# Kernel tuning notes

Hardware: AMD Instinct MI355X
Metric: run time of the kernel (lower is better)

## Reference

```python
import jax, jax.numpy as jnp
import numpy as np

# anchor encoding indices: [x,y,z,log w,log l,log h,sin,cos,vx,vy,vz]
NUM_HEADS = 8
LN_EPS = 1e-5


def layer_norm(x, g, b):
    mu = jnp.mean(x, axis=-1, keepdims=True)
    var = jnp.var(x, axis=-1, keepdims=True)
    return (x - mu) * jax.lax.rsqrt(var + LN_EPS) * g + b


def align_anchors_to_frame(anchor, Tm):
    # anchor: (..., N, 11), Tm: (..., 4, 4)
    R = Tm[..., :3, :3]
    t = Tm[..., :3, 3]
    center = jnp.einsum('...ij,...nj->...ni', R, anchor[..., 0:3]) + t[..., None, :]
    size = anchor[..., 3:6]
    yaw = jnp.einsum('...ij,...nj->...ni', R[..., :2, :2], anchor[..., 6:8])
    vel = jnp.einsum('...ij,...nj->...ni', R, anchor[..., 8:11])
    return jnp.concatenate([center, size, yaw, vel], axis=-1)


def setup_inputs() -> dict:
    key = jax.random.key(0)
    ks = jax.random.split(key, 12)
    B, T, N, C, E, A = 2, 12, 1024, 256, 256, 11
    inp = {
        'seq_features': jax.random.normal(ks[0], (B, T, N, C), jnp.float32),
        'seq_anchors': jax.random.normal(ks[1], (B, T, N, A), jnp.float32),
        'T_ego_his2cur': jax.random.normal(ks[2], (B, T, 4, 4), jnp.float32),
        'Wf': jax.random.normal(ks[3], (E, C), jnp.float32) * (C ** -0.5),
        'bf': jnp.zeros((E,), jnp.float32),
        'Wa': jax.random.normal(ks[4], (E, A), jnp.float32) * (A ** -0.5),
        'ba': jnp.zeros((E,), jnp.float32),
        'Win': jax.random.normal(ks[5], (3 * E, E), jnp.float32) * (E ** -0.5),
        'bin_': jnp.zeros((3 * E,), jnp.float32),
        'gamma': jnp.ones((E,), jnp.float32),
        'beta': jnp.zeros((E,), jnp.float32),
    }
    return inp


def reference(seq_features, seq_anchors, T_ego_his2cur, Wf, bf, Wa, ba, Win, bin_, gamma, beta):
    B, T, N, C = seq_features.shape
    E = gamma.shape[0]
    H = NUM_HEADS
    D = E // H

    feat_cur = seq_features[:, 1:]    # (B,T-1,N,C)
    feat_prev = seq_features[:, :-1]
    anc_cur = seq_anchors[:, 1:]
    anc_prev = align_anchors_to_frame(seq_anchors[:, :-1], T_ego_his2cur[:, 1:])

    tok_cur = layer_norm(feat_cur @ Wf.T + bf + anc_cur @ Wa.T + ba, gamma, beta)
    tok_prev = layer_norm(feat_prev @ Wf.T + bf + anc_prev @ Wa.T + ba, gamma, beta)

    Wq, Wk = Win[:E], Win[E:2 * E]
    bq, bk = bin_[:E], bin_[E:2 * E]
    scale = np.float32(D) ** np.float32(-0.5)
    q = ((tok_cur @ Wq.T + bq) * scale).reshape(B, T - 1, N, H, D)
    k = (tok_prev @ Wk.T + bk).reshape(B, T - 1, N, H, D)

    scores = jnp.einsum('btnhd,btmhd->bthnm', q, k)  # (B,T-1,H,N,N)
    attn = jax.nn.softmax(scores, axis=-1).mean(axis=2)  # head-averaged weights

    eye = jnp.broadcast_to(jnp.eye(N, dtype=seq_features.dtype), (B, 1, N, N))
    return jnp.concatenate([eye, attn], axis=1)  # (B,T,N,N)
```

## Files before the change

kernel.cpp:

```cpp
#include <hip/hip_runtime.h>
#include <hip/hip_bf16.h>
#include <math.h>

#define LN_EPS 1e-5f

typedef short bf16x8 __attribute__((ext_vector_type(8)));
typedef float f32x4 __attribute__((ext_vector_type(4)));

__device__ inline short f2bf(float f) {
  union { float f; unsigned u; } v; v.f = f;
  unsigned r = v.u + 0x7FFFu + ((v.u >> 16) & 1u);
  return (short)(r >> 16);
}
__device__ inline float bf2f(unsigned short s) {
  union { unsigned u; float f; } v; v.u = ((unsigned)s) << 16;
  return v.f;
}
__device__ inline float fast_exp2(float x) {
#if __has_builtin(__builtin_amdgcn_exp2f)
  return __builtin_amdgcn_exp2f(x);
#else
  return __expf(x * 0.69314718056f);
#endif
}

__global__ __launch_bounds__(256) void gemm_feat(const float* __restrict__ Ap,
    const float* __restrict__ W, const float* __restrict__ bias,
    short* __restrict__ Out)
{
  __shared__ short lda[64][40];
  __shared__ short ldb[64][40];
  const int tid = threadIdx.x;
  const int bm = blockIdx.x * 64, bn = blockIdx.y * 64;
  const int wid = tid >> 6, lane = tid & 63;
  const int quad = lane >> 4, l15 = lane & 15;
  const int wm = (wid & 1) * 32, wn = (wid >> 1) * 32;
  const int srow = tid >> 2, sseg = tid & 3;

  f32x4 z = {0.f, 0.f, 0.f, 0.f};
  f32x4 acc[2][2];
  acc[0][0] = z; acc[0][1] = z; acc[1][0] = z; acc[1][1] = z;

  for (int kk = 0; kk < 256; kk += 32) {
    {
      const float* ap = Ap + (size_t)(bm + srow) * 256 + kk + sseg * 8;
      f32x4 x0 = *(const f32x4*)ap;
      f32x4 x1 = *(const f32x4*)(ap + 4);
      bf16x8 vv;
      vv[0] = f2bf(x0[0]); vv[1] = f2bf(x0[1]); vv[2] = f2bf(x0[2]); vv[3] = f2bf(x0[3]);
      vv[4] = f2bf(x1[0]); vv[5] = f2bf(x1[1]); vv[6] = f2bf(x1[2]); vv[7] = f2bf(x1[3]);
      *(bf16x8*)&lda[srow][sseg * 8] = vv;
    }
    {
      const float* wp = W + (size_t)(bn + srow) * 256 + kk + sseg * 8;
      f32x4 x0 = *(const f32x4*)wp;
      f32x4 x1 = *(const f32x4*)(wp + 4);
      bf16x8 vv;
      vv[0] = f2bf(x0[0]); vv[1] = f2bf(x0[1]); vv[2] = f2bf(x0[2]); vv[3] = f2bf(x0[3]);
      vv[4] = f2bf(x1[0]); vv[5] = f2bf(x1[1]); vv[6] = f2bf(x1[2]); vv[7] = f2bf(x1[3]);
      *(bf16x8*)&ldb[srow][sseg * 8] = vv;
    }
    __syncthreads();
    bf16x8 af0 = *(const bf16x8*)&lda[wm + l15][quad * 8];
    bf16x8 af1 = *(const bf16x8*)&lda[wm + 16 + l15][quad * 8];
    bf16x8 bq0 = *(const bf16x8*)&ldb[wn + l15][quad * 8];
    bf16x8 bq1 = *(const bf16x8*)&ldb[wn + 16 + l15][quad * 8];
    acc[0][0] = __builtin_amdgcn_mfma_f32_16x16x32_bf16(af0, bq0, acc[0][0], 0, 0, 0);
    acc[0][1] = __builtin_amdgcn_mfma_f32_16x16x32_bf16(af0, bq1, acc[0][1], 0, 0, 0);
    acc[1][0] = __builtin_amdgcn_mfma_f32_16x16x32_bf16(af1, bq0, acc[1][0], 0, 0, 0);
    acc[1][1] = __builtin_amdgcn_mfma_f32_16x16x32_bf16(af1, bq1, acc[1][1], 0, 0, 0);
    __syncthreads();
  }

  #pragma unroll
  for (int i = 0; i < 2; ++i)
    #pragma unroll
    for (int j = 0; j < 2; ++j)
      #pragma unroll
      for (int r = 0; r < 4; ++r) {
        int grow = bm + wm + i * 16 + quad * 4 + r;
        int gcol = bn + wn + j * 16 + l15;
        Out[(size_t)grow * 256 + gcol] = f2bf(acc[i][j][r] + bias[gcol]);
      }
}

__global__ __launch_bounds__(256) void gemm_qk(const short* __restrict__ tokc,
    const short* __restrict__ tokp, const float* __restrict__ Win,
    const float* __restrict__ binv, short* __restrict__ qb, short* __restrict__ kb)
{
  const int sel = blockIdx.z;
  const short* Ap = sel ? tokp : tokc;
  const float* W = Win + (size_t)sel * 65536;
  const float* bias = binv + sel * 256;
  const float alpha = sel ? 1.0f : 0.17677669529663687f * 1.4426950408889634f;
  short* Out = sel ? kb : qb;

  __shared__ short lda[64][40];
  __shared__ short ldb[64][40];
  const int tid = threadIdx.x;
  const int bm = blockIdx.x * 64, bn = blockIdx.y * 64;
  const int wid = tid >> 6, lane = tid & 63;
  const int quad = lane >> 4, l15 = lane & 15;
  const int wm = (wid & 1) * 32, wn = (wid >> 1) * 32;
  const int srow = tid >> 2, sseg = tid & 3;

  f32x4 z = {0.f, 0.f, 0.f, 0.f};
  f32x4 acc[2][2];
  acc[0][0] = z; acc[0][1] = z; acc[1][0] = z; acc[1][1] = z;

  for (int kk = 0; kk < 256; kk += 32) {
    *(bf16x8*)&lda[srow][sseg * 8] =
        *(const bf16x8*)(Ap + (size_t)(bm + srow) * 256 + kk + sseg * 8);
    {
      const float* wp = W + (size_t)(bn + srow) * 256 + kk + sseg * 8;
      f32x4 x0 = *(const f32x4*)wp;
      f32x4 x1 = *(const f32x4*)(wp + 4);
      bf16x8 vv;
      vv[0] = f2bf(x0[0]); vv[1] = f2bf(x0[1]); vv[2] = f2bf(x0[2]); vv[3] = f2bf(x0[3]);
      vv[4] = f2bf(x1[0]); vv[5] = f2bf(x1[1]); vv[6] = f2bf(x1[2]); vv[7] = f2bf(x1[3]);
      *(bf16x8*)&ldb[srow][sseg * 8] = vv;
    }
    __syncthreads();
    bf16x8 af0 = *(const bf16x8*)&lda[wm + l15][quad * 8];
    bf16x8 af1 = *(const bf16x8*)&lda[wm + 16 + l15][quad * 8];
    bf16x8 bq0 = *(const bf16x8*)&ldb[wn + l15][quad * 8];
    bf16x8 bq1 = *(const bf16x8*)&ldb[wn + 16 + l15][quad * 8];
    acc[0][0] = __builtin_amdgcn_mfma_f32_16x16x32_bf16(af0, bq0, acc[0][0], 0, 0, 0);
    acc[0][1] = __builtin_amdgcn_mfma_f32_16x16x32_bf16(af0, bq1, acc[0][1], 0, 0, 0);
    acc[1][0] = __builtin_amdgcn_mfma_f32_16x16x32_bf16(af1, bq0, acc[1][0], 0, 0, 0);
    acc[1][1] = __builtin_amdgcn_mfma_f32_16x16x32_bf16(af1, bq1, acc[1][1], 0, 0, 0);
    __syncthreads();
  }

  #pragma unroll
  for (int i = 0; i < 2; ++i)
    #pragma unroll
    for (int j = 0; j < 2; ++j)
      #pragma unroll
      for (int r = 0; r < 4; ++r) {
        int grow = bm + wm + i * 16 + quad * 4 + r;
        int gcol = bn + wn + j * 16 + l15;
        float v = (acc[i][j][r] + bias[gcol]) * alpha;
        int btr = grow >> 10, nn = grow & 1023, h = gcol >> 5, d = gcol & 31;
        Out[(((size_t)btr * 8 + h) * 1024 + nn) * 32 + d] = f2bf(v);
      }
}

__global__ __launch_bounds__(256) void anchor_ln(const short* __restrict__ featproj,
  const float* __restrict__ anchors, const float* __restrict__ Tego,
  const float* __restrict__ Wa, const float* __restrict__ ba,
  const float* __restrict__ gamma, const float* __restrict__ beta,
  short* __restrict__ tok_cur, short* __restrict__ tok_prev)
{
  const int wid = threadIdx.x >> 6, lane = threadIdx.x & 63;
  const int tok = blockIdx.x * 4 + wid;
  const int which = tok >= 22528 ? 1 : 0;
  const int rem = tok - which * 22528;
  const int bt = rem >> 10;
  const int n = rem & 1023;
  const int b = bt / 11, t = bt - b * 11;
  const int tt = which ? t : t + 1;

  const float* ap = anchors + (((size_t)b * 12 + tt) * 1024 + n) * 11;
  float a[11];
  #pragma unroll
  for (int j = 0; j < 11; ++j) a[j] = ap[j];
  if (which) {
    const float* Tm = Tego + ((size_t)b * 12 + t + 1) * 16;
    float r00 = Tm[0], r01 = Tm[1], r02 = Tm[2],  t0 = Tm[3];
    float r10 = Tm[4], r11 = Tm[5], r12 = Tm[6],  t1 = Tm[7];
    float r20 = Tm[8], r21 = Tm[9], r22 = Tm[10], t2 = Tm[11];
    float a0 = a[0], a1 = a[1], a2 = a[2];
    float a6 = a[6], a7 = a[7], a8 = a[8], a9 = a[9], a10 = a[10];
    a[0] = r00 * a0 + r01 * a1 + r02 * a2 + t0;
    a[1] = r10 * a0 + r11 * a1 + r12 * a2 + t1;
    a[2] = r20 * a0 + r21 * a1 + r22 * a2 + t2;
    a[6] = r00 * a6 + r01 * a7;
    a[7] = r10 * a6 + r11 * a7;
    a[8] = r00 * a8 + r01 * a9 + r02 * a10;
    a[9] = r10 * a8 + r11 * a9 + r12 * a10;
    a[10] = r20 * a8 + r21 * a9 + r22 * a10;
  }

  const int c0 = lane * 4;
  const size_t frow = (((size_t)b * 12 + tt) * 1024 + n) * 256 + c0;
  ushort4 raw = *(const ushort4*)(featproj + frow);
  f32x4 bav = *(const f32x4*)(ba + c0);
  float v[4];
  v[0] = bf2f(raw.x) + bav[0]; v[1] = bf2f(raw.y) + bav[1];
  v[2] = bf2f(raw.z) + bav[2]; v[3] = bf2f(raw.w) + bav[3];
  #pragma unroll
  for (int c = 0; c < 4; ++c) {
    const float* war = Wa + (size_t)(c0 + c) * 11;
    float acc = 0.f;
    #pragma unroll
    for (int j = 0; j < 11; ++j) acc += war[j] * a[j];
    v[c] += acc;
  }
  float s1 = v[0] + v[1] + v[2] + v[3];
  float s2 = v[0]*v[0] + v[1]*v[1] + v[2]*v[2] + v[3]*v[3];
  #pragma unroll
  for (int off = 1; off < 64; off <<= 1) { s1 += __shfl_xor(s1, off); s2 += __shfl_xor(s2, off); }
  float mean = s1 * (1.0f / 256.0f);
  float var = s2 * (1.0f / 256.0f) - mean * mean;
  float rstd = rsqrtf(var + LN_EPS);
  f32x4 gv = *(const f32x4*)(gamma + c0);
  f32x4 bv = *(const f32x4*)(beta + c0);
  ushort4 o;
  o.x = (unsigned short)f2bf((v[0] - mean) * rstd * gv[0] + bv[0]);
  o.y = (unsigned short)f2bf((v[1] - mean) * rstd * gv[1] + bv[1]);
  o.z = (unsigned short)f2bf((v[2] - mean) * rstd * gv[2] + bv[2]);
  o.w = (unsigned short)f2bf((v[3] - mean) * rstd * gv[3] + bv[3]);
  short* dst = which ? tok_prev : tok_cur;
  *(ushort4*)(dst + ((size_t)bt * 1024 + n) * 256 + c0) = o;
}

__global__ __launch_bounds__(256) void denom_kernel(const short* __restrict__ q,
  const short* __restrict__ k, float* __restrict__ dinv)
{
  const int tid = threadIdx.x, wid = tid >> 6, lane = tid & 63;
  const int quad = lane >> 4, l15 = lane & 15;
  const int h = blockIdx.y, bt = blockIdx.z;
  const int n0 = blockIdx.x * 64 + wid * 16;
  const size_t base = ((size_t)bt * 8 + h) * 1024 * 32;
  bf16x8 qf = *(const bf16x8*)(q + base + (size_t)(n0 + l15) * 32 + quad * 8);
  const short* kbp = k + base;
  f32x4 z = {0.f, 0.f, 0.f, 0.f};
  float sum0 = 0, sum1 = 0, sum2 = 0, sum3 = 0;
  for (int m0 = 0; m0 < 1024; m0 += 16) {
    bf16x8 kf = *(const bf16x8*)(kbp + (size_t)(m0 + l15) * 32 + quad * 8);
    f32x4 s = __builtin_amdgcn_mfma_f32_16x16x32_bf16(qf, kf, z, 0, 0, 0);
    sum0 += fast_exp2(s[0]); sum1 += fast_exp2(s[1]);
    sum2 += fast_exp2(s[2]); sum3 += fast_exp2(s[3]);
  }
  #pragma unroll
  for (int off = 1; off < 16; off <<= 1) {
    sum0 += __shfl_xor(sum0, off); sum1 += __shfl_xor(sum1, off);
    sum2 += __shfl_xor(sum2, off); sum3 += __shfl_xor(sum3, off);
  }
  if (l15 == 0) {
    float* dp = dinv + ((size_t)bt * 8 + h) * 1024 + n0 + quad * 4;
    dp[0] = 1.f / sum0; dp[1] = 1.f / sum1; dp[2] = 1.f / sum2; dp[3] = 1.f / sum3;
  }
}

__global__ __launch_bounds__(256) void prob_kernel(const short* __restrict__ q,
  const short* __restrict__ k, const float* __restrict__ dinv, float* __restrict__ out)
{
  const int tid = threadIdx.x, wid = tid >> 6, lane = tid & 63;
  const int quad = lane >> 4, l15 = lane & 15;
  const int bt = blockIdx.z;
  const int n0 = blockIdx.x * 64 + wid * 16;
  const int mbase = blockIdx.y * 128;
  const int b = bt / 11, t = bt - b * 11;
  bf16x8 qf[8];
  float invd[8][4];
  #pragma unroll
  for (int h = 0; h < 8; ++h) {
    const size_t base = ((size_t)bt * 8 + h) * 1024 * 32;
    qf[h] = *(const bf16x8*)(q + base + (size_t)(n0 + l15) * 32 + quad * 8);
    const float* dp = dinv + ((size_t)bt * 8 + h) * 1024 + n0 + quad * 4;
    #pragma unroll
    for (int r = 0; r < 4; ++r) invd[h][r] = dp[r] * 0.125f;
  }
  float* ob = out + ((size_t)(b * 12 + t + 1)) * 1024 * 1024;
  f32x4 z = {0.f, 0.f, 0.f, 0.f};
  for (int m0 = mbase; m0 < mbase + 128; m0 += 16) {
    float P0 = 0, P1 = 0, P2 = 0, P3 = 0;
    #pragma unroll
    for (int h = 0; h < 8; ++h) {
      const short* kbp = k + ((size_t)bt * 8 + h) * 1024 * 32;
      bf16x8 kf = *(const bf16x8*)(kbp + (size_t)(m0 + l15) * 32 + quad * 8);
      f32x4 s = __builtin_amdgcn_mfma_f32_16x16x32_bf16(qf[h], kf, z, 0, 0, 0);
      P0 += fast_exp2(s[0]) * invd[h][0];
      P1 += fast_exp2(s[1]) * invd[h][1];
      P2 += fast_exp2(s[2]) * invd[h][2];
      P3 += fast_exp2(s[3]) * invd[h][3];
    }
    float* op = ob + (size_t)(n0 + quad * 4) * 1024 + m0 + l15;
    op[0] = P0; op[1024] = P1; op[2048] = P2; op[3072] = P3;
  }
}

__global__ __launch_bounds__(256) void eye_kernel(float* __restrict__ out) {
  int gid = blockIdx.x * 256 + threadIdx.x;
  int b = gid >> 18, rem = gid & 262143;
  int n = rem >> 8, m4 = rem & 255;
  f32x4 v = {0.f, 0.f, 0.f, 0.f};
  int c = n - m4 * 4;
  if (c >= 0 && c < 4) v[c] = 1.0f;
  *(f32x4*)(out + (size_t)b * 12582912 + (size_t)n * 1024 + m4 * 4) = v;
}

extern "C" void kernel_launch(void* const* d_in, const int* in_sizes, int n_in,
                              void* d_out, int out_size, void* d_ws, size_t ws_size,
                              hipStream_t stream)
{
  const float* sf   = (const float*)d_in[0];
  const float* sa   = (const float*)d_in[1];
  const float* te   = (const float*)d_in[2];
  const float* Wf   = (const float*)d_in[3];
  const float* bfv  = (const float*)d_in[4];
  const float* Wa   = (const float*)d_in[5];
  const float* ba   = (const float*)d_in[6];
  const float* Win  = (const float*)d_in[7];
  const float* binv = (const float*)d_in[8];
  const float* gam  = (const float*)d_in[9];
  const float* bet  = (const float*)d_in[10];
  float* out = (float*)d_out;

  char* w = (char*)d_ws;
  short* featproj = (short*)w;  w += 12582912;
  short* tok_cur  = (short*)w;  w += 11534336;
  short* tok_prev = (short*)w;  w += 11534336;
  short* qb       = (short*)w;  w += 11534336;
  short* kb       = (short*)w;  w += 11534336;
  float* dinv     = (float*)w;  w += 720896;

  gemm_feat<<<dim3(384, 4), 256, 0, stream>>>(sf, Wf, bfv, featproj);
  anchor_ln<<<dim3(11264), 256, 0, stream>>>(featproj, sa, te, Wa, ba, gam, bet, tok_cur, tok_prev);
  gemm_qk<<<dim3(352, 4, 2), 256, 0, stream>>>(tok_cur, tok_prev, Win, binv, qb, kb);
  denom_kernel<<<dim3(16, 8, 22), 256, 0, stream>>>(qb, kb, dinv);
  prob_kernel<<<dim3(16, 8, 22), 256, 0, stream>>>(qb, kb, dinv, out);
  eye_kernel<<<dim3(2048), 256, 0, stream>>>(out);
}
```

Baseline: 301.4 us.

## Stage K tiles through double-buffered LDS in denom and prob kernels

Both the denominator and probability kernels now load K cooperatively into a double-buffered shared-memory tile, prefetching the next tile into registers while the current one is consumed, instead of every wave reading K straight from global memory. The four waves in a block share each K tile, which should cut redundant global or L2 traffic. In exchange it adds two block-wide barriers per iteration and uses 16 KB of LDS per block, which could reduce occupancy and serialize waves. The prob kernel's main cost is probably the large fp32 output write, so the gain there may be limited.

```diff
diff --git a/kernel.cpp b/kernel.cpp
--- a/kernel.cpp
+++ b/kernel.cpp
@@ -218,20 +218,42 @@
 __global__ __launch_bounds__(256) void denom_kernel(const short* __restrict__ q,
   const short* __restrict__ k, float* __restrict__ dinv)
 {
+  __shared__ short kst[2][4096];
   const int tid = threadIdx.x, wid = tid >> 6, lane = tid & 63;
   const int quad = lane >> 4, l15 = lane & 15;
   const int h = blockIdx.y, bt = blockIdx.z;
   const int n0 = blockIdx.x * 64 + wid * 16;
   const size_t base = ((size_t)bt * 8 + h) * 1024 * 32;
   bf16x8 qf = *(const bf16x8*)(q + base + (size_t)(n0 + l15) * 32 + quad * 8);
-  const short* kbp = k + base;
+  const short* ksA = k + base + (size_t)(wid * 16) * 32 + lane * 8;
+  const short* ksB = k + base + (size_t)((wid + 4) * 16) * 32 + lane * 8;
+  short* lwA = &kst[0][wid * 512 + lane * 8];
+  short* lwB = &kst[0][(wid + 4) * 512 + lane * 8];
+
   f32x4 z = {0.f, 0.f, 0.f, 0.f};
   float sum0 = 0, sum1 = 0, sum2 = 0, sum3 = 0;
-  for (int m0 = 0; m0 < 1024; m0 += 16) {
-    bf16x8 kf = *(const bf16x8*)(kbp + (size_t)(m0 + l15) * 32 + quad * 8);
-    f32x4 s = __builtin_amdgcn_mfma_f32_16x16x32_bf16(qf, kf, z, 0, 0, 0);
-    sum0 += fast_exp2(s[0]); sum1 += fast_exp2(s[1]);
-    sum2 += fast_exp2(s[2]); sum3 += fast_exp2(s[3]);
+
+  bf16x8 stA = *(const bf16x8*)ksA;
+  bf16x8 stB = *(const bf16x8*)ksB;
+
+  #pragma unroll 1
+  for (int rd = 0; rd < 8; ++rd) {
+    const int buf = rd & 1;
+    *(bf16x8*)(lwA + buf * 4096) = stA;
+    *(bf16x8*)(lwB + buf * 4096) = stB;
+    __syncthreads();
+    if (rd < 7) {
+      stA = *(const bf16x8*)(ksA + (size_t)(rd + 1) * 128 * 32);
+      stB = *(const bf16x8*)(ksB + (size_t)(rd + 1) * 128 * 32);
+    }
+    #pragma unroll
+    for (int s = 0; s < 8; ++s) {
+      bf16x8 kf = *(const bf16x8*)&kst[buf][s * 512 + l15 * 32 + quad * 8];
+      f32x4 sc = __builtin_amdgcn_mfma_f32_16x16x32_bf16(qf, kf, z, 0, 0, 0);
+      sum0 += fast_exp2(sc[0]); sum1 += fast_exp2(sc[1]);
+      sum2 += fast_exp2(sc[2]); sum3 += fast_exp2(sc[3]);
+    }
+    __syncthreads();
   }
   #pragma unroll
   for (int off = 1; off < 16; off <<= 1) {
@@ -247,6 +269,7 @@
 __global__ __launch_bounds__(256) void prob_kernel(const short* __restrict__ q,
   const short* __restrict__ k, const float* __restrict__ dinv, float* __restrict__ out)
 {
+  __shared__ short kst[2][4096];
   const int tid = threadIdx.x, wid = tid >> 6, lane = tid & 63;
   const int quad = lane >> 4, l15 = lane & 15;
   const int bt = blockIdx.z;
@@ -263,22 +286,41 @@
     #pragma unroll
     for (int r = 0; r < 4; ++r) invd[h][r] = dp[r] * 0.125f;
   }
-  float* ob = out + ((size_t)(b * 12 + t + 1)) * 1024 * 1024;
+  const short* ksA = k + (((size_t)bt * 8 + wid    ) * 1024 + mbase) * 32 + lane * 8;
+  const short* ksB = k + (((size_t)bt * 8 + wid + 4) * 1024 + mbase) * 32 + lane * 8;
+  short* lwA = &kst[0][wid * 512 + lane * 8];
+  short* lwB = &kst[0][(wid + 4) * 512 + lane * 8];
+
+  float* ob = out + ((size_t)(b * 12 + t + 1)) * 1024 * 1024
+                  + (size_t)(n0 + quad * 4) * 1024 + l15;
   f32x4 z = {0.f, 0.f, 0.f, 0.f};
-  for (int m0 = mbase; m0 < mbase + 128; m0 += 16) {
+
+  bf16x8 stA = *(const bf16x8*)ksA;
+  bf16x8 stB = *(const bf16x8*)ksB;
+
+  #pragma unroll 1
+  for (int mt = 0; mt < 8; ++mt) {
+    const int buf = mt & 1;
+    *(bf16x8*)(lwA + buf * 4096) = stA;
+    *(bf16x8*)(lwB + buf * 4096) = stB;
+    __syncthreads();
+    if (mt < 7) {
+      stA = *(const bf16x8*)(ksA + (size_t)(mt + 1) * 16 * 32);
+      stB = *(const bf16x8*)(ksB + (size_t)(mt + 1) * 16 * 32);
+    }
     float P0 = 0, P1 = 0, P2 = 0, P3 = 0;
     #pragma unroll
     for (int h = 0; h < 8; ++h) {
-      const short* kbp = k + ((size_t)bt * 8 + h) * 1024 * 32;
-      bf16x8 kf = *(const bf16x8*)(kbp + (size_t)(m0 + l15) * 32 + quad * 8);
+      bf16x8 kf = *(const bf16x8*)&kst[buf][h * 512 + l15 * 32 + quad * 8];
       f32x4 s = __builtin_amdgcn_mfma_f32_16x16x32_bf16(qf[h], kf, z, 0, 0, 0);
       P0 += fast_exp2(s[0]) * invd[h][0];
       P1 += fast_exp2(s[1]) * invd[h][1];
       P2 += fast_exp2(s[2]) * invd[h][2];
       P3 += fast_exp2(s[3]) * invd[h][3];
     }
-    float* op = ob + (size_t)(n0 + quad * 4) * 1024 + m0 + l15;
+    float* op = ob + mbase + mt * 16;
     op[0] = P0; op[1024] = P1; op[2048] = P2; op[3072] = P3;
+    __syncthreads();
   }
 }
 
```

Result: faster. 271.6 us (-9.9%).
